# Kernel tuning notes

Hardware: AMD Instinct MI355X
Metric: run time of the kernel (lower is better)

## Reference

```python
import jax, jax.numpy as jnp
import numpy as np

K_SIZE = 3            # kernel_size
PAD = K_SIZE // 2     # zero padding on each side
EPS = 1e-5            # torch layer_norm default eps


def setup_inputs() -> dict:
    key = jax.random.key(0)
    ks = jax.random.split(key, 9)
    B, C, H, W = 4, 256, 64, 64
    Cout = 256
    sc = 1.0 / np.sqrt(C)
    return {
        "x":  jax.random.normal(ks[0], (B, C, H, W), dtype=jnp.float32),
        "Wq": jax.random.normal(ks[1], (C, C), dtype=jnp.float32) * sc,
        "bq": jax.random.normal(ks[2], (C,), dtype=jnp.float32) * 0.02,
        "Wk": jax.random.normal(ks[3], (C, C), dtype=jnp.float32) * sc,
        "bk": jax.random.normal(ks[4], (C,), dtype=jnp.float32) * 0.02,
        "Wv": jax.random.normal(ks[5], (C, C), dtype=jnp.float32) * sc,
        "bv": jax.random.normal(ks[6], (C,), dtype=jnp.float32) * 0.02,
        "Wo": jax.random.normal(ks[7], (C, Cout), dtype=jnp.float32) * sc,
        "bo": jax.random.normal(ks[8], (Cout,), dtype=jnp.float32) * 0.02,
    }


def _forward(x, Wq, bq, Wk, bk, Wv, bv, Wo, bo):
    B, C, H, W = x.shape
    # F.layer_norm(x, [H, W]): normalize over last two dims per (b, c), no affine
    mean = jnp.mean(x, axis=(2, 3), keepdims=True)
    var = jnp.var(x, axis=(2, 3), keepdims=True)
    xn = (x - mean) * jax.lax.rsqrt(var + EPS)
    # zero pad spatial dims
    p = jnp.pad(xn, ((0, 0), (0, 0), (PAD, PAD), (PAD, PAD)))
    # channels-last for per-pixel linears
    p = jnp.transpose(p, (0, 2, 3, 1))          # [B, Hp, Wp, C]
    xc = jnp.transpose(xn, (0, 2, 3, 1))        # [B, H,  W,  C] (window centers)
    scale = jnp.asarray(C, x.dtype) ** -0.5     # depth_scale = C**-0.5
    q = (xc @ Wq + bq) * scale                  # [B, H, W, C] (center-token query)
    kf = p @ Wk + bk                            # [B, Hp, Wp, C]
    vf = p @ Wv + bv
    # gather the kk=9 shifted views -> window tokens per pixel
    Kw = jnp.stack([kf[:, dh:dh + H, dw:dw + W, :]
                    for dh in range(K_SIZE) for dw in range(K_SIZE)], axis=3)  # [B,H,W,kk,C]
    Vw = jnp.stack([vf[:, dh:dh + H, dw:dw + W, :]
                    for dh in range(K_SIZE) for dw in range(K_SIZE)], axis=3)
    logits = jnp.einsum('bhwc,bhwnc->bhwn', q, Kw)     # [B, H, W, kk]
    attn = jax.nn.softmax(logits, axis=-1)
    ctx = jnp.einsum('bhwn,bhwnc->bhwc', attn, Vw)     # [B, H, W, C]
    out = ctx @ Wo + bo                                # [B, H, W, Cout]
    return jnp.transpose(out, (0, 3, 1, 2))            # [B, Cout, H, W]


def reference(x, Wq, bq, Wk, bk, Wv, bv, Wo, bo):
    return _forward(x, Wq, bq, Wk, bk, Wv, bv, Wo, bo)
```

## Files before the change

kernel.cpp:

```cpp
#include <hip/hip_runtime.h>
#include <hip/hip_bf16.h>
#include <stdint.h>

typedef __bf16 bf16x8 __attribute__((ext_vector_type(8)));
typedef float f32x4 __attribute__((ext_vector_type(4)));

#define KDIM 256
#define NPIX 16384
#define QKVS 768

__device__ __forceinline__ float b2f(ushort u){
    union { float f; uint32_t i; } x; x.i = ((uint32_t)u) << 16; return x.f;
}
__device__ __forceinline__ ushort f2b(float f){
    uint32_t u = __float_as_uint(f);
    uint32_t r = (u + 0x7fffu + ((u >> 16) & 1u)) >> 16;
    return (ushort)r;
}
__device__ __forceinline__ void unpack2(uint d, float& lo, float& hi){
    lo = __uint_as_float(d << 16);
    hi = __uint_as_float(d & 0xffff0000u);
}
__device__ __forceinline__ uint cvtpk(float lo, float hi){
    uint r;
    asm volatile("v_cvt_pk_bf16_f32 %0, %1, %2" : "=v"(r) : "v"(lo), "v"(hi));
    return r;
}

__global__ __launch_bounds__(256)
void ln_fuse(const float* __restrict__ x, ushort* __restrict__ xt,
             float* __restrict__ psum, float* __restrict__ psum2){
    __shared__ ushort sh[128 * 68];
    __shared__ float ssum[16 * 132], ssum2[16 * 132];
    const int bid = blockIdx.x;
    const int b = bid >> 7, rem = bid & 127, h = rem >> 1, ch = (rem & 1) * 128;
    const int tid = threadIdx.x;
    const int csub = tid >> 4, w4 = tid & 15;
#pragma unroll
    for (int i = 0; i < 8; ++i){
        int c = csub + 16 * i;
        float4 v = *(const float4*)(x + ((size_t)(b * 256 + ch + c)) * 4096
                                      + h * 64 + w4 * 4);
        ushort4 u; u.x = f2b(v.x); u.y = f2b(v.y); u.z = f2b(v.z); u.w = f2b(v.w);
        *(ushort4*)&sh[c * 68 + w4 * 4] = u;
        ssum [w4 * 132 + c] = v.x + v.y + v.z + v.w;
        ssum2[w4 * 132 + c] = v.x * v.x + v.y * v.y + v.z * v.z + v.w * v.w;
    }
    __syncthreads();
    if (tid < 128){
        float S = 0.f, S2 = 0.f;
#pragma unroll
        for (int j = 0; j < 16; ++j){ S += ssum[j * 132 + tid]; S2 += ssum2[j * 132 + tid]; }
        psum [(b * 64 + h) * 256 + ch + tid] = S;
        psum2[(b * 64 + h) * 256 + ch + tid] = S2;
    }
    const int c16 = tid & 15, w16 = tid >> 4;
#pragma unroll
    for (int p = 0; p < 4; ++p){
        int w = p * 16 + w16;
        union { ushort u[8]; uint4 v; } r;
#pragma unroll
        for (int j = 0; j < 8; ++j) r.u[j] = sh[(c16 * 8 + j) * 68 + w];
        size_t row = (size_t)(b * 4096 + h * 64 + w);
        *(uint4*)(xt + row * 256 + ch + c16 * 8) = r.v;
    }
}

__global__ __launch_bounds__(256)
void prep2(const float* __restrict__ Wq, const float* __restrict__ bq,
           const float* __restrict__ Wk, const float* __restrict__ bk,
           const float* __restrict__ Wv, const float* __restrict__ bv,
           const float* __restrict__ Wo,
           const float* __restrict__ psum, const float* __restrict__ psum2,
           ushort* __restrict__ wtq, ushort* __restrict__ wot,
           float* __restrict__ biasp, ushort* __restrict__ qkv){
    __shared__ float shW[32 * 33];
    __shared__ float shS[8 * 32], shS2[8 * 32], shRV[4 * 32], shM[256];
    const int bid = blockIdx.x, tid = threadIdx.x;
    if (bid < 192){
        int mat = bid / 64, tile = bid % 64;
        int ti = tile & 7, tj = tile >> 3;
        {
            int kk = tid & 31, idx = tid >> 5;
            int b = idx >> 1, h0 = (idx & 1) * 32;
            float S = 0.f, S2 = 0.f;
            for (int r = 0; r < 32; ++r){
                int off = (b * 64 + h0 + r) * 256 + tj * 32 + kk;
                S += psum[off]; S2 += psum2[off];
            }
            shS[idx * 32 + kk] = S; shS2[idx * 32 + kk] = S2;
        }
        __syncthreads();
        if (tid < 128){
            int b = tid >> 5, kk = tid & 31;
            float S  = shS [(b * 2) * 32 + kk] + shS [(b * 2 + 1) * 32 + kk];
            float S2 = shS2[(b * 2) * 32 + kk] + shS2[(b * 2 + 1) * 32 + kk];
            float m = S * (1.f / 4096.f);
            float v = S2 * (1.f / 4096.f) - m * m;
            shRV[b * 32 + kk] = rsqrtf(v + 1e-5f);
        }
        const float* src = (mat == 0) ? Wq : (mat == 1) ? Wk : Wv;
        float qs = (mat == 0) ? 0.0625f : 1.0f;
        int tx = tid & 31, ty = tid >> 5;
#pragma unroll
        for (int i = 0; i < 4; ++i)
            shW[(ty + i * 8) * 33 + tx] =
                src[(size_t)(tj * 32 + ty + i * 8) * 256 + ti * 32 + tx] * qs;
        __syncthreads();
#pragma unroll
        for (int b = 0; b < 4; ++b){
            float rv = shRV[b * 32 + tx];
#pragma unroll
            for (int i = 0; i < 4; ++i){
                int n = mat * 256 + ti * 32 + ty + i * 8;
                wtq[((size_t)b * 768 + n) * 256 + tj * 32 + tx] =
                    f2b(shW[tx * 33 + ty + i * 8] * rv);
            }
        }
    } else if (bid < 256){
        int tile = bid - 192;
        int ti = tile & 7, tj = tile >> 3;
        int tx = tid & 31, ty = tid >> 5;
#pragma unroll
        for (int i = 0; i < 4; ++i)
            shW[(ty + i * 8) * 33 + tx] =
                Wo[(size_t)(tj * 32 + ty + i * 8) * 256 + ti * 32 + tx];
        __syncthreads();
#pragma unroll
        for (int i = 0; i < 4; ++i)
            wot[(size_t)(ti * 32 + ty + i * 8) * 256 + tj * 32 + tx] =
                f2b(shW[tx * 33 + ty + i * 8]);
    } else if (bid < 268){
        int t = bid - 256;
        int b = t / 3, mat = t % 3;
        float S = 0.f, S2 = 0.f;
        for (int h = 0; h < 64; ++h){
            S += psum[(b * 64 + h) * 256 + tid]; S2 += psum2[(b * 64 + h) * 256 + tid];
        }
        float m = S * (1.f / 4096.f);
        float v = S2 * (1.f / 4096.f) - m * m;
        shM[tid] = m * rsqrtf(v + 1e-5f);
        __syncthreads();
        const float* W  = (mat == 0) ? Wq : (mat == 1) ? Wk : Wv;
        const float* bb = (mat == 0) ? bq : (mat == 1) ? bk : bv;
        float qs = (mat == 0) ? 0.0625f : 1.0f;
        float acc = 0.f;
        for (int c = 0; c < 256; ++c)
            acc += shM[c] * W[(size_t)c * 256 + tid];
        biasp[b * 768 + mat * 256 + tid] = (bb[tid] - acc) * qs;
    } else {
        ushort* pad = qkv + (size_t)NPIX * QKVS;
        pad[tid]       = 0;
        pad[256 + tid] = f2b(bk[tid]);
        pad[512 + tid] = f2b(bv[tid]);
    }
}

__global__ __launch_bounds__(512, 1)
void gemm_qkv(const ushort* __restrict__ X, const ushort* __restrict__ Y,
              const float* __restrict__ bias, ushort* __restrict__ zb){
    __shared__ ushort ldsA[2][256 * 64];
    __shared__ ushort ldsB[2][256 * 64];
    const int tid  = threadIdx.x;
    const int lane = tid & 63;
    const int wid  = tid >> 6;
    const int wm   = wid >> 2;
    const int wn   = wid & 3;
    const int id    = blockIdx.x;
    const int mtile = id & 63, ntile = id >> 6;
    const int x0 = mtile * 256, y0 = ntile * 256;
    const int bsel = x0 >> 12;
    const ushort* Yb   = Y + ((size_t)bsel * QKVS + y0) * 256;
    const float* biasb = bias + bsel * QKVS;

    auto stage = [&](int buf, int k0){
#pragma unroll
        for (int i = 0; i < 4; ++i){
            int f   = i * 512 + tid;
            int row = f >> 3, cp = f & 7;
            int cs  = cp ^ (row & 7);
            const ushort* ga = X  + (size_t)(x0 + row) * KDIM + k0 + cs * 8;
            const ushort* gb = Yb + (size_t)row        * KDIM + k0 + cs * 8;
            __builtin_amdgcn_global_load_lds(
                (const __attribute__((address_space(1))) void*)ga,
                (__attribute__((address_space(3))) void*)&ldsA[buf][f * 8], 16, 0, 0);
            __builtin_amdgcn_global_load_lds(
                (const __attribute__((address_space(1))) void*)gb,
                (__attribute__((address_space(3))) void*)&ldsB[buf][f * 8], 16, 0, 0);
        }
    };

    f32x4 acc[8][4];
#pragma unroll
    for (int i = 0; i < 8; ++i)
#pragma unroll
        for (int j = 0; j < 4; ++j) acc[i][j] = f32x4{0.f, 0.f, 0.f, 0.f};

    stage(0, 0);
    stage(1, 64);
#pragma unroll
    for (int t = 0; t < 4; ++t){
        if (t < 3) asm volatile("s_waitcnt vmcnt(8)" ::: "memory");
        else       asm volatile("s_waitcnt vmcnt(0)" ::: "memory");
        __builtin_amdgcn_sched_barrier(0);
        __builtin_amdgcn_s_barrier();
        __builtin_amdgcn_sched_barrier(0);
        const int buf = t & 1;
        __builtin_amdgcn_s_setprio(1);
#pragma unroll
        for (int kk = 0; kk < 2; ++kk){
            bf16x8 af[8], bf[4];
#pragma unroll
            for (int fm = 0; fm < 8; ++fm){
                int r = wm * 128 + fm * 16 + (lane & 15);
                int c = kk * 4 + (lane >> 4);
                af[fm] = *(const bf16x8*)&ldsA[buf][(r * 8 + (c ^ (r & 7))) * 8];
            }
#pragma unroll
            for (int fn = 0; fn < 4; ++fn){
                int r = wn * 64 + fn * 16 + (lane & 15);
                int c = kk * 4 + (lane >> 4);
                bf[fn] = *(const bf16x8*)&ldsB[buf][(r * 8 + (c ^ (r & 7))) * 8];
            }
#pragma unroll
            for (int fm = 0; fm < 8; ++fm)
#pragma unroll
                for (int fn = 0; fn < 4; ++fn)
                    acc[fm][fn] = __builtin_amdgcn_mfma_f32_16x16x32_bf16(
                        af[fm], bf[fn], acc[fm][fn], 0, 0, 0);
        }
        __builtin_amdgcn_s_setprio(0);
        __builtin_amdgcn_sched_barrier(0);
        __builtin_amdgcn_s_barrier();
        __builtin_amdgcn_sched_barrier(0);
        if (t < 2) stage(t & 1, (t + 2) * 64);
    }

#pragma unroll
    for (int fm = 0; fm < 8; ++fm){
#pragma unroll
        for (int fn = 0; fn < 4; ++fn){
            int xr = x0 + wm * 128 + fm * 16 + ((lane >> 4) << 2);
            int yc = y0 + wn * 64 + fn * 16 + (lane & 15);
            float bv = biasb[yc];
#pragma unroll
            for (int r = 0; r < 4; ++r)
                zb[(size_t)(xr + r) * QKVS + yc] = f2b(acc[fm][fn][r] + bv);
        }
    }
}

__global__ __launch_bounds__(512, 4)
void attn_out2(const ushort* __restrict__ qkv, const ushort* __restrict__ wot,
               const float* __restrict__ bo, float* __restrict__ out){
    __shared__ ushort ctx[32 * 256];
    const int tid = threadIdx.x;
    const int lane = tid & 63, wid = tid >> 6;
    const int l16 = lane & 15, pg = lane >> 4;
    const int p = wid * 4 + pg;
    const int pix = blockIdx.x * 32 + p;
    const int b = pix >> 12, hw = pix & 4095;
    const int h = hw >> 6, w = hw & 63;
    const uint PADOFF = (uint)NPIX * QKVS;
    const int cbase = l16 * 16;

    const ushort* qp = qkv + (size_t)pix * QKVS + cbase;
    uint4 qa = *(const uint4*)qp;
    uint4 qb = *(const uint4*)(qp + 8);
    float qf[16];
    unpack2(qa.x, qf[0], qf[1]);  unpack2(qa.y, qf[2], qf[3]);
    unpack2(qa.z, qf[4], qf[5]);  unpack2(qa.w, qf[6], qf[7]);
    unpack2(qb.x, qf[8], qf[9]);  unpack2(qb.y, qf[10], qf[11]);
    unpack2(qb.z, qf[12], qf[13]); unpack2(qb.w, qf[14], qf[15]);

    float lg[9];
    uint roff[9];
#pragma unroll
    for (int n = 0; n < 9; ++n){
        int nh = h + n / 3 - 1, nw = w + n % 3 - 1;
        bool ok = ((unsigned)nh < 64u) & ((unsigned)nw < 64u);
        roff[n] = ok ? (uint)(((b << 12) + (nh << 6) + nw) * QKVS) : PADOFF;
        const ushort* kp = qkv + roff[n] + 256 + cbase;
        uint4 ka = *(const uint4*)kp;
        uint4 kb = *(const uint4*)(kp + 8);
        float kf[16];
        unpack2(ka.x, kf[0], kf[1]);  unpack2(ka.y, kf[2], kf[3]);
        unpack2(ka.z, kf[4], kf[5]);  unpack2(ka.w, kf[6], kf[7]);
        unpack2(kb.x, kf[8], kf[9]);  unpack2(kb.y, kf[10], kf[11]);
        unpack2(kb.z, kf[12], kf[13]); unpack2(kb.w, kf[14], kf[15]);
        float d = 0.f;
#pragma unroll
        for (int j = 0; j < 16; ++j) d += qf[j] * kf[j];
        d += __shfl_xor(d, 1); d += __shfl_xor(d, 2);
        d += __shfl_xor(d, 4); d += __shfl_xor(d, 8);
        lg[n] = d;
    }
    float m = lg[0];
#pragma unroll
    for (int n = 1; n < 9; ++n) m = fmaxf(m, lg[n]);
    float e[9], s = 0.f;
#pragma unroll
    for (int n = 0; n < 9; ++n){ e[n] = __expf(lg[n] - m); s += e[n]; }
    float inv = 1.f / s;

    float c[16];
#pragma unroll
    for (int j = 0; j < 16; ++j) c[j] = 0.f;
#pragma unroll
    for (int n = 0; n < 9; ++n){
        float a = e[n] * inv;
        const ushort* vp = qkv + roff[n] + 512 + cbase;
        uint4 va = *(const uint4*)vp;
        uint4 vb = *(const uint4*)(vp + 8);
        float vf[16];
        unpack2(va.x, vf[0], vf[1]);  unpack2(va.y, vf[2], vf[3]);
        unpack2(va.z, vf[4], vf[5]);  unpack2(va.w, vf[6], vf[7]);
        unpack2(vb.x, vf[8], vf[9]);  unpack2(vb.y, vf[10], vf[11]);
        unpack2(vb.z, vf[12], vf[13]); unpack2(vb.w, vf[14], vf[15]);
#pragma unroll
        for (int j = 0; j < 16; ++j) c[j] += a * vf[j];
    }
    uint4 oa, ob;
    oa.x = cvtpk(c[0], c[1]);   oa.y = cvtpk(c[2], c[3]);
    oa.z = cvtpk(c[4], c[5]);   oa.w = cvtpk(c[6], c[7]);
    ob.x = cvtpk(c[8], c[9]);   ob.y = cvtpk(c[10], c[11]);
    ob.z = cvtpk(c[12], c[13]); ob.w = cvtpk(c[14], c[15]);
    *(uint4*)&ctx[p * 256 + (((l16 * 2)     ^ (p & 7)) * 8)] = oa;
    *(uint4*)&ctx[p * 256 + (((l16 * 2 + 1) ^ (p & 7)) * 8)] = ob;
    __syncthreads();

    f32x4 acc2[2][2];
    acc2[0][0] = f32x4{0,0,0,0}; acc2[0][1] = f32x4{0,0,0,0};
    acc2[1][0] = f32x4{0,0,0,0}; acc2[1][1] = f32x4{0,0,0,0};
#pragma unroll
    for (int kk = 0; kk < 8; ++kk){
        const int ck = kk * 4 + (lane >> 4);
        bf16x8 af[2], bf[2];
#pragma unroll
        for (int fm = 0; fm < 2; ++fm){
            int r = wid * 32 + fm * 16 + (lane & 15);
            af[fm] = *(const bf16x8*)(wot + (size_t)r * 256 + ck * 8);
        }
#pragma unroll
        for (int fn = 0; fn < 2; ++fn){
            int pr = fn * 16 + (lane & 15);
            bf[fn] = *(const bf16x8*)&ctx[pr * 256 + ((ck ^ (pr & 7)) * 8)];
        }
#pragma unroll
        for (int fm = 0; fm < 2; ++fm)
#pragma unroll
            for (int fn = 0; fn < 2; ++fn)
                acc2[fm][fn] = __builtin_amdgcn_mfma_f32_16x16x32_bf16(
                    af[fm], bf[fn], acc2[fm][fn], 0, 0, 0);
    }

    const int bblk = (blockIdx.x * 32) >> 12;
    const int hwb  = (blockIdx.x * 32) & 4095;
#pragma unroll
    for (int fm = 0; fm < 2; ++fm){
#pragma unroll
        for (int fn = 0; fn < 2; ++fn){
            int ch0   = wid * 32 + fm * 16 + ((lane >> 4) << 2);
            int wpix  = fn * 16 + (lane & 15);
#pragma unroll
            for (int r = 0; r < 4; ++r){
                int ch = ch0 + r;
                out[((size_t)(bblk * 256 + ch)) * 4096 + hwb + wpix] =
                    acc2[fm][fn][r] + bo[ch];
            }
        }
    }
}

extern "C" void kernel_launch(void* const* d_in, const int* in_sizes, int n_in,
                              void* d_out, int out_size, void* d_ws, size_t ws_size,
                              hipStream_t stream){
    const float* x  = (const float*)d_in[0];
    const float* Wq = (const float*)d_in[1];
    const float* bq = (const float*)d_in[2];
    const float* Wk = (const float*)d_in[3];
    const float* bk = (const float*)d_in[4];
    const float* Wv = (const float*)d_in[5];
    const float* bv = (const float*)d_in[6];
    const float* Wo = (const float*)d_in[7];
    const float* bo = (const float*)d_in[8];
    float* out = (float*)d_out;

    char* ws = (char*)d_ws;
    ushort* wtq    = (ushort*)(ws);
    ushort* wot    = (ushort*)(ws + 1572864);
    float*  biasp  = (float*) (ws + 1703936);
    float*  psum   = (float*) (ws + 1716224);
    float*  psum2  = (float*) (ws + 1978368);
    ushort* xt     = (ushort*)(ws + 2240512);
    ushort* qkv    = (ushort*)(ws + 10629120);

    ln_fuse<<<512, 256, 0, stream>>>(x, xt, psum, psum2);
    prep2<<<269, 256, 0, stream>>>(Wq, bq, Wk, bk, Wv, bv, Wo,
                                   psum, psum2, wtq, wot, biasp, qkv);

    gemm_qkv<<<192, 512, 0, stream>>>(xt, wtq, biasp, qkv);

    attn_out2<<<512, 512, 0, stream>>>(qkv, wot, bo, out);
}
```

Measured before the change: 59.04 us.

## Fold output projection into value weights and drop the attention-side GEMM

Since attention weights sum to one, Wv·Wo is precomputed in a new small kernel and the V projection uses it, with the bias becoming bv·Wo. The output GEMM in the attention kernel then reduces to a transposed store plus bias. The QKV GEMM is retiled to 256x192 with 256 blocks and a remapped tile order for better CU coverage. This adds an extra launch and a 256x256x256 fp32 weight product, and changes bf16 rounding of the fused weights.

```diff
diff --git a/kernel.cpp b/kernel.cpp
--- a/kernel.cpp
+++ b/kernel.cpp
@@ -21,10 +21,22 @@
     lo = __uint_as_float(d << 16);
     hi = __uint_as_float(d & 0xffff0000u);
 }
-__device__ __forceinline__ uint cvtpk(float lo, float hi){
-    uint r;
-    asm volatile("v_cvt_pk_bf16_f32 %0, %1, %2" : "=v"(r) : "v"(lo), "v"(hi));
-    return r;
+
+__global__ __launch_bounds__(256)
+void prep0(const float* __restrict__ Wv, const float* __restrict__ Wo,
+           const float* __restrict__ bv,
+           float* __restrict__ wvo, float* __restrict__ bvwo){
+    __shared__ float sh[256];
+    const int bid = blockIdx.x, tid = threadIdx.x;
+    const float* src = (bid < 256) ? (Wv + (size_t)bid * 256) : bv;
+    sh[tid] = src[tid];
+    __syncthreads();
+    float acc = 0.f;
+#pragma unroll 8
+    for (int c = 0; c < 256; ++c)
+        acc += sh[c] * Wo[(size_t)c * 256 + tid];
+    if (bid < 256) wvo[(size_t)bid * 256 + tid] = acc;
+    else           bvwo[tid] = acc;
 }
 
 __global__ __launch_bounds__(256)
@@ -69,11 +81,10 @@
 __global__ __launch_bounds__(256)
 void prep2(const float* __restrict__ Wq, const float* __restrict__ bq,
            const float* __restrict__ Wk, const float* __restrict__ bk,
-           const float* __restrict__ Wv, const float* __restrict__ bv,
-           const float* __restrict__ Wo,
+           const float* __restrict__ wvo, const float* __restrict__ bvwo,
            const float* __restrict__ psum, const float* __restrict__ psum2,
-           ushort* __restrict__ wtq, ushort* __restrict__ wot,
-           float* __restrict__ biasp, ushort* __restrict__ qkv){
+           ushort* __restrict__ wtq, float* __restrict__ biasp,
+           ushort* __restrict__ qkv){
     __shared__ float shW[32 * 33];
     __shared__ float shS[8 * 32], shS2[8 * 32], shRV[4 * 32], shM[256];
     const int bid = blockIdx.x, tid = threadIdx.x;
@@ -99,7 +110,7 @@
             float v = S2 * (1.f / 4096.f) - m * m;
             shRV[b * 32 + kk] = rsqrtf(v + 1e-5f);
         }
-        const float* src = (mat == 0) ? Wq : (mat == 1) ? Wk : Wv;
+        const float* src = (mat == 0) ? Wq : (mat == 1) ? Wk : wvo;
         float qs = (mat == 0) ? 0.0625f : 1.0f;
         int tx = tid & 31, ty = tid >> 5;
 #pragma unroll
@@ -117,21 +128,8 @@
                     f2b(shW[tx * 33 + ty + i * 8] * rv);
             }
         }
-    } else if (bid < 256){
-        int tile = bid - 192;
-        int ti = tile & 7, tj = tile >> 3;
-        int tx = tid & 31, ty = tid >> 5;
-#pragma unroll
-        for (int i = 0; i < 4; ++i)
-            shW[(ty + i * 8) * 33 + tx] =
-                Wo[(size_t)(tj * 32 + ty + i * 8) * 256 + ti * 32 + tx];
-        __syncthreads();
-#pragma unroll
-        for (int i = 0; i < 4; ++i)
-            wot[(size_t)(ti * 32 + ty + i * 8) * 256 + tj * 32 + tx] =
-                f2b(shW[tx * 33 + ty + i * 8]);
-    } else if (bid < 268){
-        int t = bid - 256;
+    } else if (bid < 204){
+        int t = bid - 192;
         int b = t / 3, mat = t % 3;
         float S = 0.f, S2 = 0.f;
         for (int h = 0; h < 64; ++h){
@@ -141,8 +139,8 @@
         float v = S2 * (1.f / 4096.f) - m * m;
         shM[tid] = m * rsqrtf(v + 1e-5f);
         __syncthreads();
-        const float* W  = (mat == 0) ? Wq : (mat == 1) ? Wk : Wv;
-        const float* bb = (mat == 0) ? bq : (mat == 1) ? bk : bv;
+        const float* W  = (mat == 0) ? Wq : (mat == 1) ? Wk : wvo;
+        const float* bb = (mat == 0) ? bq : (mat == 1) ? bk : bvwo;
         float qs = (mat == 0) ? 0.0625f : 1.0f;
         float acc = 0.f;
         for (int c = 0; c < 256; ++c)
@@ -152,7 +150,7 @@
         ushort* pad = qkv + (size_t)NPIX * QKVS;
         pad[tid]       = 0;
         pad[256 + tid] = f2b(bk[tid]);
-        pad[512 + tid] = f2b(bv[tid]);
+        pad[512 + tid] = f2b(bvwo[tid]);
     }
 }
 
@@ -160,15 +158,15 @@
 void gemm_qkv(const ushort* __restrict__ X, const ushort* __restrict__ Y,
               const float* __restrict__ bias, ushort* __restrict__ zb){
     __shared__ ushort ldsA[2][256 * 64];
-    __shared__ ushort ldsB[2][256 * 64];
+    __shared__ ushort ldsB[2][192 * 64];
     const int tid  = threadIdx.x;
     const int lane = tid & 63;
     const int wid  = tid >> 6;
     const int wm   = wid >> 2;
     const int wn   = wid & 3;
-    const int id    = blockIdx.x;
-    const int mtile = id & 63, ntile = id >> 6;
-    const int x0 = mtile * 256, y0 = ntile * 256;
+    const int tile  = (blockIdx.x & 7) * 32 + (blockIdx.x >> 3);
+    const int mtile = tile >> 2, ntile = tile & 3;
+    const int x0 = mtile * 256, y0 = ntile * 192;
     const int bsel = x0 >> 12;
     const ushort* Yb   = Y + ((size_t)bsel * QKVS + y0) * 256;
     const float* biasb = bias + bsel * QKVS;
@@ -179,28 +177,34 @@
             int f   = i * 512 + tid;
             int row = f >> 3, cp = f & 7;
             int cs  = cp ^ (row & 7);
-            const ushort* ga = X  + (size_t)(x0 + row) * KDIM + k0 + cs * 8;
-            const ushort* gb = Yb + (size_t)row        * KDIM + k0 + cs * 8;
+            const ushort* ga = X + (size_t)(x0 + row) * KDIM + k0 + cs * 8;
             __builtin_amdgcn_global_load_lds(
                 (const __attribute__((address_space(1))) void*)ga,
                 (__attribute__((address_space(3))) void*)&ldsA[buf][f * 8], 16, 0, 0);
+        }
+#pragma unroll
+        for (int i = 0; i < 3; ++i){
+            int f   = i * 512 + tid;
+            int row = f >> 3, cp = f & 7;
+            int cs  = cp ^ (row & 7);
+            const ushort* gb = Yb + (size_t)row * KDIM + k0 + cs * 8;
             __builtin_amdgcn_global_load_lds(
                 (const __attribute__((address_space(1))) void*)gb,
                 (__attribute__((address_space(3))) void*)&ldsB[buf][f * 8], 16, 0, 0);
         }
     };
 
-    f32x4 acc[8][4];
+    f32x4 acc[8][3];
 #pragma unroll
     for (int i = 0; i < 8; ++i)
 #pragma unroll
-        for (int j = 0; j < 4; ++j) acc[i][j] = f32x4{0.f, 0.f, 0.f, 0.f};
+        for (int j = 0; j < 3; ++j) acc[i][j] = f32x4{0.f, 0.f, 0.f, 0.f};
 
     stage(0, 0);
     stage(1, 64);
 #pragma unroll
     for (int t = 0; t < 4; ++t){
-        if (t < 3) asm volatile("s_waitcnt vmcnt(8)" ::: "memory");
+        if (t < 3) asm volatile("s_waitcnt vmcnt(7)" ::: "memory");
         else       asm volatile("s_waitcnt vmcnt(0)" ::: "memory");
         __builtin_amdgcn_sched_barrier(0);
         __builtin_amdgcn_s_barrier();
@@ -209,7 +213,7 @@
         __builtin_amdgcn_s_setprio(1);
 #pragma unroll
         for (int kk = 0; kk < 2; ++kk){
-            bf16x8 af[8], bf[4];
+            bf16x8 af[8], bf[3];
 #pragma unroll
             for (int fm = 0; fm < 8; ++fm){
                 int r = wm * 128 + fm * 16 + (lane & 15);
@@ -217,15 +221,15 @@
                 af[fm] = *(const bf16x8*)&ldsA[buf][(r * 8 + (c ^ (r & 7))) * 8];
             }
 #pragma unroll
-            for (int fn = 0; fn < 4; ++fn){
-                int r = wn * 64 + fn * 16 + (lane & 15);
+            for (int fn = 0; fn < 3; ++fn){
+                int r = wn * 48 + fn * 16 + (lane & 15);
                 int c = kk * 4 + (lane >> 4);
                 bf[fn] = *(const bf16x8*)&ldsB[buf][(r * 8 + (c ^ (r & 7))) * 8];
             }
 #pragma unroll
             for (int fm = 0; fm < 8; ++fm)
 #pragma unroll
-                for (int fn = 0; fn < 4; ++fn)
+                for (int fn = 0; fn < 3; ++fn)
                     acc[fm][fn] = __builtin_amdgcn_mfma_f32_16x16x32_bf16(
                         af[fm], bf[fn], acc[fm][fn], 0, 0, 0);
         }
@@ -239,9 +243,9 @@
 #pragma unroll
     for (int fm = 0; fm < 8; ++fm){
 #pragma unroll
-        for (int fn = 0; fn < 4; ++fn){
+        for (int fn = 0; fn < 3; ++fn){
             int xr = x0 + wm * 128 + fm * 16 + ((lane >> 4) << 2);
-            int yc = y0 + wn * 64 + fn * 16 + (lane & 15);
+            int yc = y0 + wn * 48 + fn * 16 + (lane & 15);
             float bv = biasb[yc];
 #pragma unroll
             for (int r = 0; r < 4; ++r)
@@ -250,15 +254,15 @@
     }
 }
 
-__global__ __launch_bounds__(512, 4)
-void attn_out2(const ushort* __restrict__ qkv, const ushort* __restrict__ wot,
-               const float* __restrict__ bo, float* __restrict__ out){
-    __shared__ ushort ctx[32 * 256];
+__global__ __launch_bounds__(256)
+void attn_out3(const ushort* __restrict__ qkv, const float* __restrict__ bo,
+               float* __restrict__ out){
+    __shared__ float ctxT[256 * 17];
     const int tid = threadIdx.x;
     const int lane = tid & 63, wid = tid >> 6;
     const int l16 = lane & 15, pg = lane >> 4;
     const int p = wid * 4 + pg;
-    const int pix = blockIdx.x * 32 + p;
+    const int pix = blockIdx.x * 16 + p;
     const int b = pix >> 12, hw = pix & 4095;
     const int h = hw >> 6, w = hw & 63;
     const uint PADOFF = (uint)NPIX * QKVS;
@@ -320,55 +324,19 @@
 #pragma unroll
         for (int j = 0; j < 16; ++j) c[j] += a * vf[j];
     }
-    uint4 oa, ob;
-    oa.x = cvtpk(c[0], c[1]);   oa.y = cvtpk(c[2], c[3]);
-    oa.z = cvtpk(c[4], c[5]);   oa.w = cvtpk(c[6], c[7]);
-    ob.x = cvtpk(c[8], c[9]);   ob.y = cvtpk(c[10], c[11]);
-    ob.z = cvtpk(c[12], c[13]); ob.w = cvtpk(c[14], c[15]);
-    *(uint4*)&ctx[p * 256 + (((l16 * 2)     ^ (p & 7)) * 8)] = oa;
-    *(uint4*)&ctx[p * 256 + (((l16 * 2 + 1) ^ (p & 7)) * 8)] = ob;
+
+#pragma unroll
+    for (int j = 0; j < 16; ++j)
+        ctxT[(cbase + j) * 17 + p] = c[j];
     __syncthreads();
-
-    f32x4 acc2[2][2];
-    acc2[0][0] = f32x4{0,0,0,0}; acc2[0][1] = f32x4{0,0,0,0};
-    acc2[1][0] = f32x4{0,0,0,0}; acc2[1][1] = f32x4{0,0,0,0};
-#pragma unroll
-    for (int kk = 0; kk < 8; ++kk){
-        const int ck = kk * 4 + (lane >> 4);
-        bf16x8 af[2], bf[2];
-#pragma unroll
-        for (int fm = 0; fm < 2; ++fm){
-            int r = wid * 32 + fm * 16 + (lane & 15);
-            af[fm] = *(const bf16x8*)(wot + (size_t)r * 256 + ck * 8);
-        }
-#pragma unroll
-        for (int fn = 0; fn < 2; ++fn){
-            int pr = fn * 16 + (lane & 15);
-            bf[fn] = *(const bf16x8*)&ctx[pr * 256 + ((ck ^ (pr & 7)) * 8)];
-        }
-#pragma unroll
-        for (int fm = 0; fm < 2; ++fm)
-#pragma unroll
-            for (int fn = 0; fn < 2; ++fn)
-                acc2[fm][fn] = __builtin_amdgcn_mfma_f32_16x16x32_bf16(
-                    af[fm], bf[fn], acc2[fm][fn], 0, 0, 0);
-    }
-
-    const int bblk = (blockIdx.x * 32) >> 12;
-    const int hwb  = (blockIdx.x * 32) & 4095;
-#pragma unroll
-    for (int fm = 0; fm < 2; ++fm){
-#pragma unroll
-        for (int fn = 0; fn < 2; ++fn){
-            int ch0   = wid * 32 + fm * 16 + ((lane >> 4) << 2);
-            int wpix  = fn * 16 + (lane & 15);
-#pragma unroll
-            for (int r = 0; r < 4; ++r){
-                int ch = ch0 + r;
-                out[((size_t)(bblk * 256 + ch)) * 4096 + hwb + wpix] =
-                    acc2[fm][fn][r] + bo[ch];
-            }
-        }
+    const int base = blockIdx.x * 16;
+    const int bb = base >> 12, hwb = base & 4095;
+    float* op = out + ((size_t)bb * 256) * 4096 + hwb;
+    const int p2 = tid & 15, cg = tid >> 4;
+#pragma unroll
+    for (int i = 0; i < 16; ++i){
+        int ch = i * 16 + cg;
+        op[(size_t)ch * 4096 + p2] = ctxT[ch * 17 + p2] + bo[ch];
     }
 }
 
@@ -387,19 +355,21 @@
     float* out = (float*)d_out;
 
     char* ws = (char*)d_ws;
-    ushort* wtq    = (ushort*)(ws);
-    ushort* wot    = (ushort*)(ws + 1572864);
-    float*  biasp  = (float*) (ws + 1703936);
-    float*  psum   = (float*) (ws + 1716224);
-    float*  psum2  = (float*) (ws + 1978368);
-    ushort* xt     = (ushort*)(ws + 2240512);
-    ushort* qkv    = (ushort*)(ws + 10629120);
-
+    ushort* wtq   = (ushort*)(ws);
+    float*  biasp = (float*) (ws + 1572864);
+    float*  psum  = (float*) (ws + 1585152);
+    float*  psum2 = (float*) (ws + 1847296);
+    float*  wvo   = (float*) (ws + 2109440);
+    float*  bvwo  = (float*) (ws + 2371584);
+    ushort* xt    = (ushort*)(ws + 2372608);
+    ushort* qkv   = (ushort*)(ws + 10761216);
+
+    prep0<<<257, 256, 0, stream>>>(Wv, Wo, bv, wvo, bvwo);
     ln_fuse<<<512, 256, 0, stream>>>(x, xt, psum, psum2);
-    prep2<<<269, 256, 0, stream>>>(Wq, bq, Wk, bk, Wv, bv, Wo,
-                                   psum, psum2, wtq, wot, biasp, qkv);
-
-    gemm_qkv<<<192, 512, 0, stream>>>(xt, wtq, biasp, qkv);
-
-    attn_out2<<<512, 512, 0, stream>>>(qkv, wot, bo, out);
-}
+    prep2<<<205, 256, 0, stream>>>(Wq, bq, Wk, bk, wvo, bvwo,
+                                   psum, psum2, wtq, biasp, qkv);
+
+    gemm_qkv<<<256, 512, 0, stream>>>(xt, wtq, biasp, qkv);
+
+    attn_out3<<<1024, 256, 0, stream>>>(qkv, bo, out);
+}
```

After: 61.59 us. 4.3% more time.
